# Kernel optimization log

Hardware: AMD Instinct MI355X
Metric: run time of the kernel (lower is better)

## Reference

```python
import jax, jax.numpy as jnp
import numpy as np
from jax import lax

BS, L, HID = 16, 512, 768
H, HD, NREG = 12, 64, 8
R2 = 2 * NREG


def setup_inputs() -> dict:
    key = jax.random.key(0)
    ks = jax.random.split(key, 7)
    s = 1.0 / np.sqrt(HID)
    return {
        "hidden_states": jax.random.normal(ks[0], (BS, L, HID), jnp.float32),
        "K1_w": jax.random.normal(ks[1], (H * HD, HID), jnp.float32) * s,
        "K1_b": jnp.zeros((H * HD,), jnp.float32),
        "V1_w": jax.random.normal(ks[2], (H * HD, HID), jnp.float32) * s,
        "V1_b": jnp.zeros((H * HD,), jnp.float32),
        "reading_head": jax.random.normal(ks[3], (H, HD), jnp.float32) * (1.0 / np.sqrt(HD)),
        "bidirection_weight": jnp.ones((1, 1, H, 1, R2), jnp.float32) * (1.0 / R2),
    }


def _softmax_dim1(x):
    # torch: softmax over length dim (1) plus 1/exp(max) residual term
    m = jnp.max(x, axis=1, keepdims=True)
    e = jnp.exp(x - m)
    return e / jnp.sum(e, axis=1, keepdims=True) + jnp.exp(-m)


def _cummax_idx(e):
    # torch.cummax indices over axis=1 for a bool tensor (ties -> latest index):
    # last True index so far; if no True yet, current index.
    ar = jnp.arange(e.shape[1], dtype=jnp.int32)[None, :, None]
    lt = lax.cummax(jnp.where(e, ar, jnp.int32(-1)), axis=1)
    return jnp.where(lt >= 0, lt, ar)


def reference(hidden_states, K1_w, K1_b, V1_w, V1_b, reading_head, bidirection_weight):
    bs, length, _ = hidden_states.shape
    K1 = jax.nn.relu(hidden_states @ K1_w.T + K1_b).reshape(bs, length, H, HD)
    V1 = jax.nn.relu(hidden_states @ V1_w.T + V1_b).reshape(bs, length, H, HD)

    scores = jnp.einsum("blhn,hn->blh", K1, reading_head)
    events = _softmax_dim1(scores) > (1.5 / length)  # (bs, L, H) bool; fwd==bwd for IC1

    col0 = _cummax_idx(events)  # (bs, L, H)
    rolled = jnp.roll(events, -1, axis=1)
    col1 = jnp.flip(512 - _cummax_idx(jnp.flip(rolled, axis=1)), axis=1)
    col1 = col1.at[:, 0].set(0)

    # sequential shift-register scan over length
    e_seq = jnp.moveaxis(events, 1, 0)  # (L, bs, H)
    f_seq = jnp.moveaxis(col0, 1, 0)
    b_seq = jnp.moveaxis(col1, 1, 0)
    row0 = jnp.concatenate(
        [f_seq[0][:, None], b_seq[0][:, None], jnp.zeros((bs, R2, H), jnp.int32)], axis=1
    )  # (bs, R2+2, H)

    def step(row, inp):
        e, f, b = inp
        reg = jnp.where(e[:, None, :], row[:, :-2], row[:, 2:])  # shift-in on event
        new_row = jnp.concatenate([f[:, None], b[:, None], reg], axis=1)
        return new_row, reg

    _, regs = lax.scan(step, row0, (e_seq[1:], f_seq[1:], b_seq[1:]))
    regs = jnp.concatenate([jnp.zeros((1, bs, R2, H), jnp.int32), regs], axis=0)  # (L,bs,R2,H)
    idx = jnp.moveaxis(regs, 0, 1).reshape(bs, length * R2, H)
    idx = jnp.clip(idx, 0, length - 1)

    V2 = jnp.take_along_axis(V1, idx[..., None], axis=1).reshape(bs, length, R2, H, HD)
    w = bidirection_weight.reshape(H, R2)
    return jnp.einsum("blrhd,hr->blhd", V2, w)  # (bs, L, H, HD)
```

## Files before the change

kernel.cpp:

```cpp
#include <hip/hip_runtime.h>
#include <cstdint>
#include <cstddef>

#define BSZ 16
#define LQ  512
#define HIDDIM 768
#define NH  12
#define HD  64
#define R2V 16
#define NTOT 1536
#define MTOT 8192

typedef __bf16 bf16x8 __attribute__((ext_vector_type(8)));
typedef float  f32x4  __attribute__((ext_vector_type(4)));

__device__ inline unsigned short f2bf(float x) {
    union { float f; unsigned u; } c; c.f = x;
    unsigned r = c.u + 0x7fffu + ((c.u >> 16) & 1u);
    return (unsigned short)(r >> 16);
}
__device__ inline float bfl(unsigned u) { return __uint_as_float(u << 16); }
__device__ inline float bfh(unsigned u) { return __uint_as_float(u & 0xffff0000u); }

#define NHS4 1572864
#define NW1  147456
#define NW4  294912

__global__ __launch_bounds__(256) void cast_pack(
    const float* __restrict__ hs,
    const float* __restrict__ Kw, const float* __restrict__ Vw,
    const float* __restrict__ Kb, const float* __restrict__ Vb,
    unsigned short* __restrict__ hsb, unsigned short* __restrict__ Wb,
    float* __restrict__ biasp)
{
    const int i = blockIdx.x * 256 + threadIdx.x;
    float4 v; unsigned short* dst;
    if (i < NHS4) {
        v = ((const float4*)hs)[i];
        dst = hsb + (size_t)i * 4;
    } else {
        const int j = i - NHS4;
        v = (j < NW1) ? ((const float4*)Kw)[j] : ((const float4*)Vw)[j - NW1];
        dst = Wb + (size_t)j * 4;
    }
    ushort4 o;
    o.x = f2bf(v.x); o.y = f2bf(v.y); o.z = f2bf(v.z); o.w = f2bf(v.w);
    *(ushort4*)dst = o;
    if (i < 768) { biasp[i] = Kb[i]; biasp[768 + i] = Vb[i]; }
}

#define TBM 128
#define TBN 128
#define TBK 32
#define KT  (HIDDIM / TBK)
#define ATILE (TBM * TBK)

#define GLD16(g, l) __builtin_amdgcn_global_load_lds( \
    (const __attribute__((address_space(1))) void*)(g), \
    (__attribute__((address_space(3))) void*)(l), 16, 0, 0)

__global__ __launch_bounds__(256, 3) void gemm_mfma(
    const unsigned short* __restrict__ Abf,
    const unsigned short* __restrict__ Wbf,
    const float* __restrict__ biasp,
    unsigned short* __restrict__ K1b, unsigned short* __restrict__ V1b)
{
    __shared__ unsigned short As[3][ATILE];
    __shared__ unsigned short Bs[3][ATILE];

    const int wg  = blockIdx.y * 12 + blockIdx.x;
    const int nid = (wg & 7) * 96 + (wg >> 3);
    const int bx  = nid % 12;
    const int by  = nid / 12;
    const int n0  = bx * TBN;
    const int m0  = by * TBM;

    const int tid  = threadIdx.x;
    const int wid  = tid >> 6;
    const int lane = tid & 63;
    const int wm   = (wid & 1) * 64;
    const int wn   = (wid >> 1) * 64;

    f32x4 acc[4][4] = {};

    const int srow = lane >> 2;
    const int scol = ((lane & 3) ^ ((lane >> 3) & 3)) << 3;
    const int r0   = wid * 32;

    const unsigned short* Ag = Abf + (size_t)(m0 + r0 + srow) * HIDDIM + scol;
    const unsigned short* Bg = Wbf + (size_t)(n0 + r0 + srow) * HIDDIM + scol;

#define STAGE(buf, kt) do {                                                   \
        const int kof_ = (kt) * TBK;                                          \
        GLD16(Ag + kof_,               &As[buf][r0 * TBK]);                   \
        GLD16(Ag + 16 * HIDDIM + kof_, &As[buf][(r0 + 16) * TBK]);            \
        GLD16(Bg + kof_,               &Bs[buf][r0 * TBK]);                   \
        GLD16(Bg + 16 * HIDDIM + kof_, &Bs[buf][(r0 + 16) * TBK]);            \
    } while (0)

    const int fm   = lane & 15;
    const int fj   = lane >> 4;
    const int koff = ((fj ^ ((fm >> 1) & 3)) << 3);

    STAGE(0, 0);
    STAGE(1, 1);

    for (int kt = 0; kt < KT; ++kt) {
        if (kt < KT - 1) asm volatile("s_waitcnt vmcnt(4)" ::: "memory");
        else             asm volatile("s_waitcnt vmcnt(0)" ::: "memory");
        __builtin_amdgcn_s_barrier();
        __builtin_amdgcn_sched_barrier(0);
        if (kt + 2 < KT) STAGE((kt + 2) % 3, kt + 2);
        const int cb = kt % 3;

        bf16x8 af[4], bfr[4];
        #pragma unroll
        for (int mi = 0; mi < 4; ++mi)
            af[mi] = *reinterpret_cast<const bf16x8*>(
                &As[cb][(wm + mi * 16 + fm) * TBK + koff]);
        #pragma unroll
        for (int ni = 0; ni < 4; ++ni)
            bfr[ni] = *reinterpret_cast<const bf16x8*>(
                &Bs[cb][(wn + ni * 16 + fm) * TBK + koff]);
        __builtin_amdgcn_s_setprio(1);
        #pragma unroll
        for (int mi = 0; mi < 4; ++mi)
            #pragma unroll
            for (int ni = 0; ni < 4; ++ni)
                acc[mi][ni] = __builtin_amdgcn_mfma_f32_16x16x32_bf16(
                    bfr[ni], af[mi], acc[mi][ni], 0, 0, 0);
        __builtin_amdgcn_s_setprio(0);
    }
#undef STAGE

    const bool isK = (n0 < HIDDIM);
    unsigned short* __restrict__ dst = isK ? K1b : V1b;
    const int nsub = isK ? 0 : HIDDIM;
    const int nq   = fj * 4;

    #pragma unroll
    for (int mi = 0; mi < 4; ++mi) {
        const int mg = m0 + wm + mi * 16 + fm;
        #pragma unroll
        for (int ni = 0; ni < 4; ++ni) {
            const int ng = n0 + wn + ni * 16 + nq;
            float4 bv = *(const float4*)(biasp + ng);
            f32x4 a = acc[mi][ni];
            ushort4 o;
            o.x = f2bf(fmaxf(a[0] + bv.x, 0.f));
            o.y = f2bf(fmaxf(a[1] + bv.y, 0.f));
            o.z = f2bf(fmaxf(a[2] + bv.z, 0.f));
            o.w = f2bf(fmaxf(a[3] + bv.w, 0.f));
            *(ushort4*)(dst + (size_t)mg * HIDDIM + (ng - nsub)) = o;
        }
    }
}

#define SINF (1 << 30)
#define IXP 17

__global__ __launch_bounds__(512) void scan_gather(
    const unsigned short* __restrict__ K1b,
    const unsigned short* __restrict__ V1b,
    const float* __restrict__ rh,
    const float* __restrict__ bw,
    float* __restrict__ out)
{
    const int bh   = blockIdx.x >> 2;
    const int part = blockIdx.x & 3;
    const int b    = bh / NH;
    const int h    = bh % NH;
    const int l    = threadIdx.x;
    const int lane = l & 63;
    const int wid  = l >> 6;

    __shared__ float wredA[8];
    __shared__ float wredB[8];
    __shared__ int   wp0[8];
    __shared__ int   wp1[8];
    __shared__ int   wp2[8];
    __shared__ int   ev[LQ];
    __shared__ int   col0[LQ];
    __shared__ int   col1[LQ];
    __shared__ int   E[LQ];
    __shared__ int   idxs[LQ * IXP];
    __shared__ float wsm[R2V];

    if (l < R2V) wsm[l] = bw[h * R2V + l];

    const unsigned short* krow = K1b + ((size_t)(b * LQ + l)) * HIDDIM + h * HD;
    const float* rrow = rh + h * HD;
    float s = 0.f;
    #pragma unroll
    for (int c8 = 0; c8 < 8; ++c8) {
        uint4 kv = *(const uint4*)(krow + c8 * 8);
        float4 ra = *(const float4*)(rrow + c8 * 8);
        float4 rb = *(const float4*)(rrow + c8 * 8 + 4);
        s += bfl(kv.x) * ra.x + bfh(kv.x) * ra.y
           + bfl(kv.y) * ra.z + bfh(kv.y) * ra.w
           + bfl(kv.z) * rb.x + bfh(kv.z) * rb.y
           + bfl(kv.w) * rb.z + bfh(kv.w) * rb.w;
    }

    float mx = s;
    #pragma unroll
    for (int off = 32; off > 0; off >>= 1) mx = fmaxf(mx, __shfl_xor(mx, off));
    if (lane == 0) wredA[wid] = mx;
    __syncthreads();
    float m = wredA[0];
    #pragma unroll
    for (int i = 1; i < 8; ++i) m = fmaxf(m, wredA[i]);

    const float e = expf(s - m);
    float sm = e;
    #pragma unroll
    for (int off = 32; off > 0; off >>= 1) sm += __shfl_xor(sm, off);
    if (lane == 0) wredB[wid] = sm;
    __syncthreads();
    float ssum = 0.f;
    #pragma unroll
    for (int i = 0; i < 8; ++i) ssum += wredB[i];

    const float p = e / ssum + expf(-m);
    const int event = (p > (1.5f / 512.0f)) ? 1 : 0;
    ev[l] = event;

    int v = event ? l : -1;
    #pragma unroll
    for (int off = 1; off < 64; off <<= 1) {
        int u = __shfl_up(v, off);
        if (lane >= off) v = (u > v) ? u : v;
    }
    if (lane == 63) wp0[wid] = v;
    __syncthreads();
    int pfx = -1;
    for (int i = 0; i < wid; ++i) pfx = (wp0[i] > pfx) ? wp0[i] : pfx;
    v = (pfx > v) ? pfx : v;
    col0[l] = (v >= 0) ? v : l;

    int v1 = ev[(l + 1) & (LQ - 1)] ? l : SINF;
    #pragma unroll
    for (int off = 1; off < 64; off <<= 1) {
        int u = __shfl_down(v1, off);
        if (lane < 64 - off) v1 = (u < v1) ? u : v1;
    }
    if (lane == 0) wp1[wid] = v1;
    __syncthreads();
    int sfx = SINF;
    for (int i = wid + 1; i < 8; ++i) sfx = (wp1[i] < sfx) ? wp1[i] : sfx;
    v1 = (sfx < v1) ? sfx : v1;
    col1[l] = (l == 0) ? 0 : (((v1 < SINF) ? v1 : l) + 1);

    int c = (l >= 1) ? event : 0;
    #pragma unroll
    for (int off = 1; off < 64; off <<= 1) {
        int u = __shfl_up(c, off);
        if (lane >= off) c += u;
    }
    if (lane == 63) wp2[wid] = c;
    __syncthreads();
    for (int i = 0; i < wid; ++i) c += wp2[i];

    if (l >= 1 && event) E[c - 1] = l;
    __syncthreads();

    int* op = &idxs[l * IXP];
    #pragma unroll
    for (int j = 0; j < 8; ++j) {
        const int k = c - 1 - j;
        int f = 0, bb = 0;
        if (k >= 0) {
            const int t = E[k];
            f  = col0[t - 1];
            bb = col1[t - 1];
        }
        op[2 * j]     = min(max(f, 0), LQ - 1);
        op[2 * j + 1] = min(max(bb, 0), LQ - 1);
    }
    __syncthreads();

    const int dsl = lane & 7;
    const size_t vbase = (size_t)b * LQ * HIDDIM + h * HD + dsl * 8;

    for (int rr = 0; rr < 2; ++rr) {
        const int round = part * 2 + rr;
        const int lg = round * 64 + wid * 8 + (lane >> 3);
        const int* ip = &idxs[lg * IXP];
        float a0 = 0.f, a1 = 0.f, a2 = 0.f, a3 = 0.f;
        float a4 = 0.f, a5 = 0.f, a6 = 0.f, a7 = 0.f;
        #pragma unroll 1
        for (int rc = 0; rc < R2V; rc += 4) {
            const int i0 = ip[rc], i1 = ip[rc + 1], i2 = ip[rc + 2], i3 = ip[rc + 3];
            uint4 v0 = *(const uint4*)(V1b + vbase + (size_t)i0 * HIDDIM);
            uint4 vA = *(const uint4*)(V1b + vbase + (size_t)i1 * HIDDIM);
            uint4 vB = *(const uint4*)(V1b + vbase + (size_t)i2 * HIDDIM);
            uint4 vC = *(const uint4*)(V1b + vbase + (size_t)i3 * HIDDIM);
            const float w0 = wsm[rc], w1 = wsm[rc + 1], w2 = wsm[rc + 2], w3 = wsm[rc + 3];
            a0 += w0 * bfl(v0.x); a1 += w0 * bfh(v0.x);
            a2 += w0 * bfl(v0.y); a3 += w0 * bfh(v0.y);
            a4 += w0 * bfl(v0.z); a5 += w0 * bfh(v0.z);
            a6 += w0 * bfl(v0.w); a7 += w0 * bfh(v0.w);
            a0 += w1 * bfl(vA.x); a1 += w1 * bfh(vA.x);
            a2 += w1 * bfl(vA.y); a3 += w1 * bfh(vA.y);
            a4 += w1 * bfl(vA.z); a5 += w1 * bfh(vA.z);
            a6 += w1 * bfl(vA.w); a7 += w1 * bfh(vA.w);
            a0 += w2 * bfl(vB.x); a1 += w2 * bfh(vB.x);
            a2 += w2 * bfl(vB.y); a3 += w2 * bfh(vB.y);
            a4 += w2 * bfl(vB.z); a5 += w2 * bfh(vB.z);
            a6 += w2 * bfl(vB.w); a7 += w2 * bfh(vB.w);
            a0 += w3 * bfl(vC.x); a1 += w3 * bfh(vC.x);
            a2 += w3 * bfl(vC.y); a3 += w3 * bfh(vC.y);
            a4 += w3 * bfl(vC.z); a5 += w3 * bfh(vC.z);
            a6 += w3 * bfl(vC.w); a7 += w3 * bfh(vC.w);
        }
        float* po = out + ((size_t)(b * LQ + lg) * NH + h) * HD + dsl * 8;
        *(float4*)po       = make_float4(a0, a1, a2, a3);
        *((float4*)po + 1) = make_float4(a4, a5, a6, a7);
    }
}

extern "C" void kernel_launch(void* const* d_in, const int* in_sizes, int n_in,
                              void* d_out, int out_size, void* d_ws, size_t ws_size,
                              hipStream_t stream)
{
    (void)in_sizes; (void)n_in; (void)out_size; (void)ws_size;

    const float* hs = (const float*)d_in[0];
    const float* Kw = (const float*)d_in[1];
    const float* Kb = (const float*)d_in[2];
    const float* Vw = (const float*)d_in[3];
    const float* Vb = (const float*)d_in[4];
    const float* rh = (const float*)d_in[5];
    const float* bw = (const float*)d_in[6];
    float* out = (float*)d_out;

    char* ws = (char*)d_ws;
    unsigned short* K1b   = (unsigned short*)(ws);
    unsigned short* V1b   = (unsigned short*)(ws + 12582912);
    unsigned short* hsb   = (unsigned short*)(ws + 25165824);
    unsigned short* Wb    = (unsigned short*)(ws + 37748736);
    float*          biasp = (float*)(ws + 40108032);

    cast_pack<<<(NHS4 + NW4) / 256, 256, 0, stream>>>(hs, Kw, Vw, Kb, Vb, hsb, Wb, biasp);

    dim3 g1(NTOT / TBN, MTOT / TBM);
    gemm_mfma<<<g1, 256, 0, stream>>>(hsb, Wb, biasp, K1b, V1b);

    scan_gather<<<BSZ * NH * 4, LQ, 0, stream>>>(K1b, V1b, rh, bw, out);
}
```

Baseline: 141.0 us.

## Fuse fp32-to-bf16 cast into GEMM tile loading, drop cast kernel

Removes the separate cast_pack kernel and has the GEMM load fp32 activations and weights directly into registers, convert them to bf16, and write swizzled tiles to LDS with a register-prefetched double buffer. This eliminates a full pass that read and wrote the 25MB input plus weights and saves one launch. In exchange, each GEMM tile re-reads fp32 data (twice the bytes of bf16) across the 12 N-tiles, and it loses the async global_load_lds triple-buffer pipeline, so it adds register pressure and conversion work inside the main loop.

```diff
diff --git a/kernel.cpp b/kernel.cpp
--- a/kernel.cpp
+++ b/kernel.cpp
@@ -22,51 +22,30 @@
 __device__ inline float bfl(unsigned u) { return __uint_as_float(u << 16); }
 __device__ inline float bfh(unsigned u) { return __uint_as_float(u & 0xffff0000u); }
 
-#define NHS4 1572864
-#define NW1  147456
-#define NW4  294912
-
-__global__ __launch_bounds__(256) void cast_pack(
-    const float* __restrict__ hs,
-    const float* __restrict__ Kw, const float* __restrict__ Vw,
-    const float* __restrict__ Kb, const float* __restrict__ Vb,
-    unsigned short* __restrict__ hsb, unsigned short* __restrict__ Wb,
-    float* __restrict__ biasp)
-{
-    const int i = blockIdx.x * 256 + threadIdx.x;
-    float4 v; unsigned short* dst;
-    if (i < NHS4) {
-        v = ((const float4*)hs)[i];
-        dst = hsb + (size_t)i * 4;
-    } else {
-        const int j = i - NHS4;
-        v = (j < NW1) ? ((const float4*)Kw)[j] : ((const float4*)Vw)[j - NW1];
-        dst = Wb + (size_t)j * 4;
-    }
-    ushort4 o;
-    o.x = f2bf(v.x); o.y = f2bf(v.y); o.z = f2bf(v.z); o.w = f2bf(v.w);
-    *(ushort4*)dst = o;
-    if (i < 768) { biasp[i] = Kb[i]; biasp[768 + i] = Vb[i]; }
-}
-
 #define TBM 128
 #define TBN 128
 #define TBK 32
 #define KT  (HIDDIM / TBK)
 #define ATILE (TBM * TBK)
 
-#define GLD16(g, l) __builtin_amdgcn_global_load_lds( \
-    (const __attribute__((address_space(1))) void*)(g), \
-    (__attribute__((address_space(3))) void*)(l), 16, 0, 0)
+#define CVT8(dstp, f0, f1) do {                                               \
+        bf16x8 t_;                                                            \
+        t_[0] = (__bf16)(f0).x; t_[1] = (__bf16)(f0).y;                       \
+        t_[2] = (__bf16)(f0).z; t_[3] = (__bf16)(f0).w;                       \
+        t_[4] = (__bf16)(f1).x; t_[5] = (__bf16)(f1).y;                       \
+        t_[6] = (__bf16)(f1).z; t_[7] = (__bf16)(f1).w;                       \
+        *reinterpret_cast<bf16x8*>(dstp) = t_;                                \
+    } while (0)
 
 __global__ __launch_bounds__(256, 3) void gemm_mfma(
-    const unsigned short* __restrict__ Abf,
-    const unsigned short* __restrict__ Wbf,
-    const float* __restrict__ biasp,
+    const float* __restrict__ hs,
+    const float* __restrict__ Kw,
+    const float* __restrict__ Vw,
+    const float* __restrict__ Kb, const float* __restrict__ Vb,
     unsigned short* __restrict__ K1b, unsigned short* __restrict__ V1b)
 {
-    __shared__ unsigned short As[3][ATILE];
-    __shared__ unsigned short Bs[3][ATILE];
+    __shared__ unsigned short As[2][ATILE];
+    __shared__ unsigned short Bs[2][ATILE];
 
     const int wg  = blockIdx.y * 12 + blockIdx.x;
     const int nid = (wg & 7) * 96 + (wg >> 3);
@@ -75,6 +54,11 @@
     const int n0  = bx * TBN;
     const int m0  = by * TBM;
 
+    const bool isK = (n0 < HIDDIM);
+    const float* __restrict__ Wsrc = isK ? Kw : Vw;
+    const int nsub = isK ? 0 : HIDDIM;
+    const int nb0  = n0 - nsub;
+
     const int tid  = threadIdx.x;
     const int wid  = tid >> 6;
     const int lane = tid & 63;
@@ -83,35 +67,52 @@
 
     f32x4 acc[4][4] = {};
 
-    const int srow = lane >> 2;
-    const int scol = ((lane & 3) ^ ((lane >> 3) & 3)) << 3;
-    const int r0   = wid * 32;
-
-    const unsigned short* Ag = Abf + (size_t)(m0 + r0 + srow) * HIDDIM + scol;
-    const unsigned short* Bg = Wbf + (size_t)(n0 + r0 + srow) * HIDDIM + scol;
-
-#define STAGE(buf, kt) do {                                                   \
-        const int kof_ = (kt) * TBK;                                          \
-        GLD16(Ag + kof_,               &As[buf][r0 * TBK]);                   \
-        GLD16(Ag + 16 * HIDDIM + kof_, &As[buf][(r0 + 16) * TBK]);            \
-        GLD16(Bg + kof_,               &Bs[buf][r0 * TBK]);                   \
-        GLD16(Bg + 16 * HIDDIM + kof_, &Bs[buf][(r0 + 16) * TBK]);            \
-    } while (0)
+    const int rr = lane >> 1;
+    const int kh = lane & 1;
+    const int r0 = wid * 32;
+    const int ra = r0 + rr;
+    const int sw = (ra >> 1) & 3;
+    const int u0 = ((2 * kh) ^ sw) * 8;
+    const int u1 = ((2 * kh + 1) ^ sw) * 8;
+
+    const float* Ag = hs   + (size_t)(m0  + ra) * HIDDIM + kh * 16;
+    const float* Bg = Wsrc + (size_t)(nb0 + ra) * HIDDIM + kh * 16;
 
     const int fm   = lane & 15;
     const int fj   = lane >> 4;
     const int koff = ((fj ^ ((fm >> 1) & 3)) << 3);
 
-    STAGE(0, 0);
-    STAGE(1, 1);
+    float4 a0, a1, a2, a3, b0, b1, b2, b3;
+
+#define LOADG(kt) do {                                                        \
+        const float4* pa_ = (const float4*)(Ag + (kt) * TBK);                 \
+        a0 = pa_[0]; a1 = pa_[1]; a2 = pa_[2]; a3 = pa_[3];                   \
+        const float4* pb_ = (const float4*)(Bg + (kt) * TBK);                 \
+        b0 = pb_[0]; b1 = pb_[1]; b2 = pb_[2]; b3 = pb_[3];                   \
+    } while (0)
+
+#define CVTWRITE(buf) do {                                                    \
+        CVT8(&As[buf][ra * TBK + u0], a0, a1);                                \
+        CVT8(&As[buf][ra * TBK + u1], a2, a3);                                \
+        CVT8(&Bs[buf][ra * TBK + u0], b0, b1);                                \
+        CVT8(&Bs[buf][ra * TBK + u1], b2, b3);                                \
+    } while (0)
+
+    LOADG(0);
+    CVTWRITE(0);
+    LOADG(1);
+    asm volatile("s_waitcnt lgkmcnt(0)" ::: "memory");
+    __builtin_amdgcn_sched_barrier(0);
 
     for (int kt = 0; kt < KT; ++kt) {
-        if (kt < KT - 1) asm volatile("s_waitcnt vmcnt(4)" ::: "memory");
-        else             asm volatile("s_waitcnt vmcnt(0)" ::: "memory");
         __builtin_amdgcn_s_barrier();
         __builtin_amdgcn_sched_barrier(0);
-        if (kt + 2 < KT) STAGE((kt + 2) % 3, kt + 2);
-        const int cb = kt % 3;
+        const int cb = kt & 1;
+
+        if (kt + 1 < KT) {
+            CVTWRITE(cb ^ 1);
+            if (kt + 2 < KT) LOADG(kt + 2);
+        }
 
         bf16x8 af[4], bfr[4];
         #pragma unroll
@@ -131,12 +132,12 @@
                     bfr[ni], af[mi], acc[mi][ni], 0, 0, 0);
         __builtin_amdgcn_s_setprio(0);
     }
-#undef STAGE
-
-    const bool isK = (n0 < HIDDIM);
+#undef LOADG
+#undef CVTWRITE
+
     unsigned short* __restrict__ dst = isK ? K1b : V1b;
-    const int nsub = isK ? 0 : HIDDIM;
-    const int nq   = fj * 4;
+    const float* __restrict__ bsrc   = isK ? Kb : Vb;
+    const int nq = fj * 4;
 
     #pragma unroll
     for (int mi = 0; mi < 4; ++mi) {
@@ -144,7 +145,7 @@
         #pragma unroll
         for (int ni = 0; ni < 4; ++ni) {
             const int ng = n0 + wn + ni * 16 + nq;
-            float4 bv = *(const float4*)(biasp + ng);
+            float4 bv = *(const float4*)(bsrc + (ng - nsub));
             f32x4 a = acc[mi][ni];
             ushort4 o;
             o.x = f2bf(fmaxf(a[0] + bv.x, 0.f));
@@ -335,16 +336,11 @@
     float* out = (float*)d_out;
 
     char* ws = (char*)d_ws;
-    unsigned short* K1b   = (unsigned short*)(ws);
-    unsigned short* V1b   = (unsigned short*)(ws + 12582912);
-    unsigned short* hsb   = (unsigned short*)(ws + 25165824);
-    unsigned short* Wb    = (unsigned short*)(ws + 37748736);
-    float*          biasp = (float*)(ws + 40108032);
-
-    cast_pack<<<(NHS4 + NW4) / 256, 256, 0, stream>>>(hs, Kw, Vw, Kb, Vb, hsb, Wb, biasp);
+    unsigned short* K1b = (unsigned short*)(ws);
+    unsigned short* V1b = (unsigned short*)(ws + 12582912);
 
     dim3 g1(NTOT / TBN, MTOT / TBM);
-    gemm_mfma<<<g1, 256, 0, stream>>>(hsb, Wb, biasp, K1b, V1b);
+    gemm_mfma<<<g1, 256, 0, stream>>>(hs, Kw, Vw, Kb, Vb, K1b, V1b);
 
     scan_gather<<<BSZ * NH * 4, LQ, 0, stream>>>(K1b, V1b, rh, bw, out);
 }
```

After: 150.7 us. 6.9% more time.

## Fuse bf16 cast into GEMM kernel with a grid-wide atomic barrier

Applied to the files above, without the earlier changes.

Merges the separate fp32-to-bf16 cast kernel into the GEMM kernel. Every block first converts a strided slice of the inputs and weights, then all blocks wait on a grid-wide barrier built from a global atomic counter before starting the MFMA GEMM. This removes one kernel launch and the gap between launches. It relies on all 768 blocks being resident at the same time (3 per CU under the launch bounds) or the barrier deadlocks, and the spin-wait adds synchronisation cost.

```diff
diff --git a/kernel.cpp b/kernel.cpp
--- a/kernel.cpp
+++ b/kernel.cpp
@@ -10,6 +10,7 @@
 #define R2V 16
 #define NTOT 1536
 #define MTOT 8192
+#define NBLK 768
 
 typedef __bf16 bf16x8 __attribute__((ext_vector_type(8)));
 typedef float  f32x4  __attribute__((ext_vector_type(4)));
@@ -22,32 +23,11 @@
 __device__ inline float bfl(unsigned u) { return __uint_as_float(u << 16); }
 __device__ inline float bfh(unsigned u) { return __uint_as_float(u & 0xffff0000u); }
 
+__device__ unsigned g_arrive = 0u;
+
 #define NHS4 1572864
 #define NW1  147456
 #define NW4  294912
-
-__global__ __launch_bounds__(256) void cast_pack(
-    const float* __restrict__ hs,
-    const float* __restrict__ Kw, const float* __restrict__ Vw,
-    const float* __restrict__ Kb, const float* __restrict__ Vb,
-    unsigned short* __restrict__ hsb, unsigned short* __restrict__ Wb,
-    float* __restrict__ biasp)
-{
-    const int i = blockIdx.x * 256 + threadIdx.x;
-    float4 v; unsigned short* dst;
-    if (i < NHS4) {
-        v = ((const float4*)hs)[i];
-        dst = hsb + (size_t)i * 4;
-    } else {
-        const int j = i - NHS4;
-        v = (j < NW1) ? ((const float4*)Kw)[j] : ((const float4*)Vw)[j - NW1];
-        dst = Wb + (size_t)j * 4;
-    }
-    ushort4 o;
-    o.x = f2bf(v.x); o.y = f2bf(v.y); o.z = f2bf(v.z); o.w = f2bf(v.w);
-    *(ushort4*)dst = o;
-    if (i < 768) { biasp[i] = Kb[i]; biasp[768 + i] = Vb[i]; }
-}
 
 #define TBM 128
 #define TBN 128
@@ -59,16 +39,52 @@
     (const __attribute__((address_space(1))) void*)(g), \
     (__attribute__((address_space(3))) void*)(l), 16, 0, 0)
 
-__global__ __launch_bounds__(256, 3) void gemm_mfma(
-    const unsigned short* __restrict__ Abf,
-    const unsigned short* __restrict__ Wbf,
-    const float* __restrict__ biasp,
+__global__ __launch_bounds__(256, 3) void fused_cast_gemm(
+    const float* __restrict__ hs,
+    const float* __restrict__ Kw, const float* __restrict__ Vw,
+    const float* __restrict__ Kb, const float* __restrict__ Vb,
+    unsigned short* __restrict__ hsb,
+    unsigned short* __restrict__ Wb,
+    float* __restrict__ biasp,
     unsigned short* __restrict__ K1b, unsigned short* __restrict__ V1b)
 {
     __shared__ unsigned short As[3][ATILE];
     __shared__ unsigned short Bs[3][ATILE];
 
-    const int wg  = blockIdx.y * 12 + blockIdx.x;
+    const int wg = blockIdx.y * 12 + blockIdx.x;
+    const int t0 = wg * 256 + threadIdx.x;
+
+    for (int it = 0; it < 10; ++it) {
+        const int i = t0 + it * (NBLK * 256);
+        if (i < NHS4 + NW4) {
+            float4 v; unsigned short* dst;
+            if (i < NHS4) {
+                v = ((const float4*)hs)[i];
+                dst = hsb + (size_t)i * 4;
+            } else {
+                const int j = i - NHS4;
+                v = (j < NW1) ? ((const float4*)Kw)[j] : ((const float4*)Vw)[j - NW1];
+                dst = Wb + (size_t)j * 4;
+            }
+            ushort4 o;
+            o.x = f2bf(v.x); o.y = f2bf(v.y); o.z = f2bf(v.z); o.w = f2bf(v.w);
+            *(ushort4*)dst = o;
+        }
+    }
+    if (t0 < 768) { biasp[t0] = Kb[t0]; biasp[768 + t0] = Vb[t0]; }
+
+    __threadfence();
+    __syncthreads();
+    if (threadIdx.x == 0) {
+        unsigned a = __hip_atomic_fetch_add(&g_arrive, 1u,
+                        __ATOMIC_ACQ_REL, __HIP_MEMORY_SCOPE_AGENT);
+        const unsigned tgt = (a / (unsigned)NBLK + 1u) * (unsigned)NBLK;
+        while (__hip_atomic_load(&g_arrive,
+                        __ATOMIC_ACQUIRE, __HIP_MEMORY_SCOPE_AGENT) < tgt)
+            __builtin_amdgcn_s_sleep(8);
+    }
+    __syncthreads();
+
     const int nid = (wg & 7) * 96 + (wg >> 3);
     const int bx  = nid % 12;
     const int by  = nid / 12;
@@ -87,8 +103,8 @@
     const int scol = ((lane & 3) ^ ((lane >> 3) & 3)) << 3;
     const int r0   = wid * 32;
 
-    const unsigned short* Ag = Abf + (size_t)(m0 + r0 + srow) * HIDDIM + scol;
-    const unsigned short* Bg = Wbf + (size_t)(n0 + r0 + srow) * HIDDIM + scol;
+    const unsigned short* Ag = hsb + (size_t)(m0 + r0 + srow) * HIDDIM + scol;
+    const unsigned short* Bg = Wb  + (size_t)(n0 + r0 + srow) * HIDDIM + scol;
 
 #define STAGE(buf, kt) do {                                                   \
         const int kof_ = (kt) * TBK;                                          \
@@ -341,10 +357,9 @@
     unsigned short* Wb    = (unsigned short*)(ws + 37748736);
     float*          biasp = (float*)(ws + 40108032);
 
-    cast_pack<<<(NHS4 + NW4) / 256, 256, 0, stream>>>(hs, Kw, Vw, Kb, Vb, hsb, Wb, biasp);
-
     dim3 g1(NTOT / TBN, MTOT / TBM);
-    gemm_mfma<<<g1, 256, 0, stream>>>(hsb, Wb, biasp, K1b, V1b);
+    fused_cast_gemm<<<g1, 256, 0, stream>>>(hs, Kw, Vw, Kb, Vb,
+                                            hsb, Wb, biasp, K1b, V1b);
 
     scan_gather<<<BSZ * NH * 4, LQ, 0, stream>>>(K1b, V1b, rh, bw, out);
 }
```

Measured after the change: 235.8 us. 67.3% more time.
